# Kernel tuning notes

Measured on AMD Instinct MI355X. Metric: run time of the kernel, lower is better.

The kernel has to match this reference:

```python
import jax, jax.numpy as jnp
import numpy as np

THRESHOLD = 0.5
NEG_POS_RATIO = 3
ALPHA = 1.0
N_CLASSES = 81


def xy_to_cxcy(xy):
    return jnp.concatenate([(xy[..., :2] + xy[..., 2:]) / 2.0,
                            xy[..., 2:] - xy[..., :2]], axis=-1)


def cxcy_to_xy(cxcy):
    return jnp.concatenate([cxcy[..., :2] - cxcy[..., 2:] / 2.0,
                            cxcy[..., :2] + cxcy[..., 2:] / 2.0], axis=-1)


def cxcy_to_gcxgcy(cxcy, priors_cxcy):
    # SSD encoding with standard variances (0.1 for center, 0.2 for size)
    g_cxcy = (cxcy[..., :2] - priors_cxcy[..., :2]) / (priors_cxcy[..., 2:] / 10.0)
    g_wh = jnp.log(cxcy[..., 2:] / priors_cxcy[..., 2:]) * 5.0
    return jnp.concatenate([g_cxcy, g_wh], axis=-1)


def iou_pairwise(a_xy, b_xy):
    # a_xy: (N, O, 4), b_xy: (P, 4) -> (N, O, P)
    lt = jnp.maximum(a_xy[..., :, None, :2], b_xy[None, None, :, :2])
    rb = jnp.minimum(a_xy[..., :, None, 2:], b_xy[None, None, :, 2:])
    wh = jnp.clip(rb - lt, 0.0)
    inter = wh[..., 0] * wh[..., 1]
    area_a = (a_xy[..., 2] - a_xy[..., 0]) * (a_xy[..., 3] - a_xy[..., 1])
    area_b = (b_xy[:, 2] - b_xy[:, 0]) * (b_xy[:, 3] - b_xy[:, 1])
    union = area_a[..., :, None] + area_b[None, None, :] - inter
    return inter / union


def setup_inputs() -> dict:
    key = jax.random.key(0)
    k1, k2, k3, k4, k5, k6, k7 = jax.random.split(key, 7)
    N, P, C, O = 32, 8732, N_CLASSES, 16
    predicted_locs = jax.random.normal(k1, (N, P, 4), dtype=jnp.float32)
    predicted_scores = jax.random.normal(k2, (N, P, C), dtype=jnp.float32)
    # ground-truth boxes: build valid cxcy then convert to xy in [0, 1]
    b_cxy = jax.random.uniform(k3, (N, O, 2), minval=0.2, maxval=0.8)
    b_wh = jax.random.uniform(k4, (N, O, 2), minval=0.05, maxval=0.3)
    boxes = cxcy_to_xy(jnp.concatenate([b_cxy, b_wh], axis=-1)).astype(jnp.float32)
    labels = jax.random.randint(k5, (N, O), 1, C).astype(jnp.int32)  # 0 = background
    # priors in cxcy, valid (positive wh)
    p_cxy = jax.random.uniform(k6, (P, 2), minval=0.05, maxval=0.95)
    p_wh = jax.random.uniform(k7, (P, 2), minval=0.05, maxval=0.4)
    priors_cxcy = jnp.concatenate([p_cxy, p_wh], axis=-1).astype(jnp.float32)
    return {"predicted_locs": predicted_locs, "predicted_scores": predicted_scores,
            "boxes": boxes, "labels": labels, "priors_cxcy": priors_cxcy}


def reference(predicted_locs, predicted_scores, boxes, labels, priors_cxcy):
    N, P, C = predicted_scores.shape
    O = boxes.shape[1]
    priors_xy = cxcy_to_xy(priors_cxcy)  # (P, 4)

    overlap = iou_pairwise(boxes, priors_xy)            # (N, O, P)
    overlap_for_each_prior = overlap.max(axis=1)        # (N, P)
    object_for_each_prior = overlap.argmax(axis=1)      # (N, P)
    prior_for_each_object = overlap.argmax(axis=2)      # (N, O)

    obj_ids = jnp.arange(O)

    def assign(ofp, ovl, pfo):
        # force each object to be matched to its best prior with overlap 1
        ofp = ofp.at[pfo].set(obj_ids)
        ovl = ovl.at[pfo].set(1.0)
        return ofp, ovl

    object_for_each_prior, overlap_for_each_prior = jax.vmap(assign)(
        object_for_each_prior, overlap_for_each_prior, prior_for_each_object)

    label_for_each_prior = jnp.take_along_axis(labels, object_for_each_prior, axis=1)  # (N, P)
    true_classes = jnp.where(overlap_for_each_prior < THRESHOLD, 0, label_for_each_prior)

    matched_boxes = jnp.take_along_axis(
        boxes, object_for_each_prior[..., None], axis=1)  # (N, P, 4)
    true_locs = cxcy_to_gcxgcy(xy_to_cxcy(matched_boxes), priors_cxcy)

    positive = true_classes != 0                          # (N, P)
    pos_f = positive.astype(predicted_locs.dtype)

    # localization loss (L1, reduction='none' in original despite the name)
    loc_per_prior = jnp.abs(predicted_locs - true_locs).sum(axis=-1)  # (N, P)
    n_pos_total = pos_f.sum()
    loc_loss = (loc_per_prior * pos_f).sum() / (4.0 * n_pos_total)

    # confidence loss (cross entropy per prior)
    logp = jax.nn.log_softmax(predicted_scores, axis=-1)
    ce = -jnp.take_along_axis(logp, true_classes[..., None], axis=-1)[..., 0]  # (N, P)

    conf_loss_pos = (ce * pos_f).sum()
    ce_neg = jnp.where(positive, 0.0, ce)
    ce_neg_sorted = -jnp.sort(-ce_neg, axis=1)            # descending
    n_positives = positive.sum(axis=1)                    # (N,)
    hard = (jnp.arange(P)[None, :] < (NEG_POS_RATIO * n_positives)[:, None]).astype(ce.dtype)
    conf_loss_hard_neg = (ce_neg_sorted * hard).sum()
    conf_loss = (conf_loss_hard_neg + conf_loss_pos) / n_pos_total

    return conf_loss + ALPHA * loc_loss
```

## Files before the change

### kernel.cpp

```cpp
#include <hip/hip_runtime.h>
#include <hip/hip_bf16.h>
#include <stdint.h>

#define BLOCK 256
#define SBLOCK 128
#define MAXO 64
#define TK_THREADS 1024
#define CK_MAX 4096

__global__ void match_object_kernel(const float* __restrict__ boxes,
                                    const float* __restrict__ priors,
                                    int* __restrict__ pfop,
                                    float* __restrict__ acc, int* __restrict__ n_pos,
                                    unsigned* __restrict__ done, int N, int P, int O) {
    __shared__ unsigned long long swm[4];
    int idx = blockIdx.x, tid = threadIdx.x;
    if (idx == 0) {
        for (int j = tid; j < N; j += BLOCK) n_pos[j] = 0;
        if (tid >= 64 && tid < 67) acc[tid - 64] = 0.f;
        if (tid == 96) *done = 0u;
    }
    const float* b = boxes + (size_t)idx * 4;
    float bx0 = b[0], by0 = b[1], bx1 = b[2], by1 = b[3];
    float areaa = (bx1 - bx0) * (by1 - by0);

    unsigned long long best = 0ULL;
    for (int p = tid; p < P; p += BLOCK) {
        float4 pr = ((const float4*)priors)[p];
        float px0 = pr.x - pr.z * 0.5f, py0 = pr.y - pr.w * 0.5f;
        float px1 = pr.x + pr.z * 0.5f, py1 = pr.y + pr.w * 0.5f;
        float areab = (px1 - px0) * (py1 - py0);
        float ltx = fmaxf(bx0, px0), lty = fmaxf(by0, py0);
        float rbx = fminf(bx1, px1), rby = fminf(by1, py1);
        float wx = fmaxf(rbx - ltx, 0.f), wy = fmaxf(rby - lty, 0.f);
        float inter = wx * wy;
        float iou = inter / (areaa + areab - inter);
        unsigned long long cand = (((unsigned long long)__float_as_uint(iou)) << 32) |
                                  (unsigned long long)(0xFFFFFFFFu - (unsigned)p);
        if (cand > best) best = cand;
    }
    #pragma unroll
    for (int off = 32; off >= 1; off >>= 1) {
        unsigned long long other = __shfl_down(best, off);
        if (other > best) best = other;
    }
    if ((tid & 63) == 0) swm[tid >> 6] = best;
    __syncthreads();
    if (tid == 0) {
        unsigned long long r = swm[0];
        for (int w = 1; w < BLOCK / 64; ++w) if (swm[w] > r) r = swm[w];
        pfop[idx] = (int)(0xFFFFFFFFu - (unsigned)(r & 0xFFFFFFFFull));
    }
}

__global__ void __launch_bounds__(SBLOCK)
fused_staged_kernel(const float* __restrict__ boxes,
                    const float* __restrict__ priors,
                    const float* __restrict__ locs,
                    const int* __restrict__ labels,
                    const int* __restrict__ pfop,
                    const float* __restrict__ scores,
                    float* __restrict__ ce_neg,
                    float* __restrict__ pb_loc, float* __restrict__ pb_pce,
                    int* __restrict__ pb_npos,
                    int N, int P, int O) {
    __shared__ float4 sstage4[SBLOCK * 81 / 4];
    __shared__ float sbx[MAXO * 4];
    __shared__ int   spf[MAXO];
    __shared__ int   slab[MAXO];
    __shared__ float sl[2], sp[2]; __shared__ int sn[2];
    const float* sstage = (const float*)sstage4;

    int n = blockIdx.y, bx = blockIdx.x, tid = threadIdx.x;
    int w = tid >> 6, lane = tid & 63;
    int p0 = bx * SBLOCK;
    int rows = P - p0; if (rows > SBLOCK) rows = SBLOCK;
    int p = p0 + tid;
    bool valid = tid < rows;
    size_t t = (size_t)n * P + p;

    for (int i = tid; i < O * 4; i += SBLOCK) sbx[i] = boxes[(size_t)n * O * 4 + i];
    for (int i = tid; i < O; i += SBLOCK) { spf[i] = pfop[n * O + i]; slab[i] = labels[n * O + i]; }
    float4 pr = make_float4(0.f, 0.f, 1.f, 1.f);
    float4 pl = make_float4(0.f, 0.f, 0.f, 0.f);
    if (valid) {
        pr = ((const float4*)priors)[p];
        pl = ((const float4*)locs)[t];
    }

    const float4* chunk = (const float4*)(scores + ((size_t)n * P + p0) * 81);
    if (rows == SBLOCK) {
        #pragma unroll
        for (int j = 0; j < 20; ++j)
            sstage4[j * SBLOCK + tid] = chunk[j * SBLOCK + tid];
        if (tid < 32)
            sstage4[20 * SBLOCK + tid] = chunk[20 * SBLOCK + tid];
    } else {
        int nf4 = rows * 81 / 4;
        for (int j = 0; j < 21; ++j) {
            int idx = j * SBLOCK + tid;
            if (idx < nf4) sstage4[idx] = chunk[idx];
        }
    }
    __syncthreads();

    float my_loc = 0.f, my_pce = 0.f; int my_pos = 0;
    if (valid) {
        const float* row = sstage + tid * 81;
        float e = 0.f;
        #pragma unroll
        for (int j = 0; j < 81; ++j) e += __expf(row[j]);

        float px0 = pr.x - pr.z * 0.5f, py0 = pr.y - pr.w * 0.5f;
        float px1 = pr.x + pr.z * 0.5f, py1 = pr.y + pr.w * 0.5f;
        float areab = (px1 - px0) * (py1 - py0);
        float best = -1.f; int bo = 0;
        for (int o = 0; o < O; ++o) {
            float x0 = sbx[o*4+0], y0 = sbx[o*4+1], x1 = sbx[o*4+2], y1 = sbx[o*4+3];
            float ltx = fmaxf(x0, px0), lty = fmaxf(y0, py0);
            float rbx = fminf(x1, px1), rby = fminf(y1, py1);
            float wx = fmaxf(rbx - ltx, 0.f), wy = fmaxf(rby - lty, 0.f);
            float inter = wx * wy;
            float areao = (x1 - x0) * (y1 - y0);
            float iou = inter / (areao + areab - inter);
            if (iou > best) { best = iou; bo = o; }
        }
        int fo = -1;
        for (int o = 0; o < O; ++o) if (spf[o] == p) fo = o;
        int obj; float ov;
        if (fo >= 0) { obj = fo; ov = 1.0f; }
        else         { obj = bo; ov = best; }
        int tc = (ov < 0.5f) ? 0 : slab[obj];

        float stc = row[tc];
        float ce = logf(e) - stc;
        bool pos = (tc != 0);
        ce_neg[t] = pos ? 0.f : ce;
        if (pos) {
            my_pce = ce; my_pos = 1;
            float x0 = sbx[obj*4+0], y0 = sbx[obj*4+1], x1 = sbx[obj*4+2], y1 = sbx[obj*4+3];
            float cx = (x0 + x1) * 0.5f, cy = (y0 + y1) * 0.5f;
            float bw = x1 - x0, bh = y1 - y0;
            float g0 = (cx - pr.x) / (pr.z / 10.0f);
            float g1 = (cy - pr.y) / (pr.w / 10.0f);
            float g2 = logf(bw / pr.z) * 5.0f;
            float g3 = logf(bh / pr.w) * 5.0f;
            my_loc = fabsf(pl.x-g0) + fabsf(pl.y-g1) + fabsf(pl.z-g2) + fabsf(pl.w-g3);
        }
    }

    #pragma unroll
    for (int off = 32; off >= 1; off >>= 1) {
        my_loc += __shfl_down(my_loc, off);
        my_pce += __shfl_down(my_pce, off);
        my_pos += __shfl_down(my_pos, off);
    }
    if (lane == 0) { sl[w] = my_loc; sp[w] = my_pce; sn[w] = my_pos; }
    __syncthreads();
    if (tid == 0) {
        int npb = gridDim.x;
        pb_loc[n * npb + bx]  = sl[0] + sl[1];
        pb_pce[n * npb + bx]  = sp[0] + sp[1];
        pb_npos[n * npb + bx] = sn[0] + sn[1];
    }
}

__global__ void match_prior_kernel(const float* __restrict__ boxes,
                                   const float* __restrict__ priors,
                                   const float* __restrict__ locs,
                                   const int* __restrict__ labels,
                                   const int* __restrict__ pfop,
                                   int* __restrict__ tcarr,
                                   float* __restrict__ acc, int* __restrict__ n_pos,
                                   int N, int P, int O) {
    __shared__ float sbx[MAXO * 4];
    __shared__ float sarea[MAXO];
    __shared__ int   spf[MAXO];
    __shared__ int   slab[MAXO];
    int n = blockIdx.y, tid = threadIdx.x;
    if (tid < O * 4) sbx[tid] = boxes[(size_t)n * O * 4 + tid];
    if (tid >= 128 && tid < 128 + O) spf[tid - 128]  = pfop[n * O + (tid - 128)];
    if (tid >= 192 && tid < 192 + O) slab[tid - 192] = labels[n * O + (tid - 192)];
    __syncthreads();
    if (tid < O)
        sarea[tid] = (sbx[tid*4+2] - sbx[tid*4+0]) * (sbx[tid*4+3] - sbx[tid*4+1]);
    __syncthreads();

    int p = blockIdx.x * BLOCK + tid;
    bool valid = p < P;
    float my_loc = 0.f; int my_pos = 0;
    if (valid) {
        float4 pr = ((const float4*)priors)[p];
        float px0 = pr.x - pr.z * 0.5f, py0 = pr.y - pr.w * 0.5f;
        float px1 = pr.x + pr.z * 0.5f, py1 = pr.y + pr.w * 0.5f;
        float areab = (px1 - px0) * (py1 - py0);

        float best = -1.f; int bo = 0;
        for (int o = 0; o < O; ++o) {
            float ltx = fmaxf(sbx[o*4+0], px0);
            float lty = fmaxf(sbx[o*4+1], py0);
            float rbx = fminf(sbx[o*4+2], px1);
            float rby = fminf(sbx[o*4+3], py1);
            float wx = fmaxf(rbx - ltx, 0.f), wy = fmaxf(rby - lty, 0.f);
            float inter = wx * wy;
            float iou = inter / (sarea[o] + areab - inter);
            if (iou > best) { best = iou; bo = o; }
        }
        int fo = -1;
        for (int o = 0; o < O; ++o) if (spf[o] == p) fo = o;
        int obj; float ov;
        if (fo >= 0) { obj = fo; ov = 1.0f; }
        else         { obj = bo; ov = best; }
        int lab = slab[obj];
        int tc = (ov < 0.5f) ? 0 : lab;
        tcarr[(size_t)n * P + p] = tc;
        if (tc != 0) {
            my_pos = 1;
            float x0 = sbx[obj*4+0], y0 = sbx[obj*4+1], x1 = sbx[obj*4+2], y1 = sbx[obj*4+3];
            float cx = (x0 + x1) * 0.5f, cy = (y0 + y1) * 0.5f;
            float w = x1 - x0, h = y1 - y0;
            float g0 = (cx - pr.x) / (pr.z / 10.0f);
            float g1 = (cy - pr.y) / (pr.w / 10.0f);
            float g2 = logf(w / pr.z) * 5.0f;
            float g3 = logf(h / pr.w) * 5.0f;
            const float* pl = locs + ((size_t)n * P + p) * 4;
            my_loc = fabsf(pl[0]-g0) + fabsf(pl[1]-g1) + fabsf(pl[2]-g2) + fabsf(pl[3]-g3);
        }
    }
    #pragma unroll
    for (int off = 32; off >= 1; off >>= 1) {
        my_loc += __shfl_down(my_loc, off);
        my_pos += __shfl_down(my_pos, off);
    }
    if ((tid & 63) == 0 && my_pos) {
        atomicAdd(&acc[0], my_loc);
        atomicAdd(&n_pos[n], my_pos);
    }
}

__global__ void loss_generic_kernel(const float* __restrict__ scores,
                                    const int* __restrict__ tcarr,
                                    float* __restrict__ ce_neg, float* __restrict__ acc,
                                    int NP, int C) {
    int t = blockIdx.x * blockDim.x + threadIdx.x;
    if (t >= NP) return;
    int tc = tcarr[t];
    const float* s = scores + (size_t)t * C;
    float m = -3.0e38f;
    for (int j = 0; j < C; ++j) m = fmaxf(m, s[j]);
    float l = 0.f, stc = 0.f;
    for (int j = 0; j < C; ++j) {
        float v = s[j];
        l += __expf(v - m);
        if (j == tc) stc = v;
    }
    float ce = m + logf(l) - stc;
    bool pos = (tc != 0);
    ce_neg[t] = pos ? 0.f : ce;
    if (pos) atomicAdd(&acc[1], ce);
}

__global__ void topk_final_kernel(const float* __restrict__ ce_neg,
                                  int* __restrict__ n_pos,
                                  const float* __restrict__ pb_loc,
                                  const float* __restrict__ pb_pce,
                                  const int* __restrict__ pb_npos, int npb,
                                  float* __restrict__ acc, unsigned* __restrict__ done,
                                  int N, int P, unsigned* __restrict__ out) {
    __shared__ unsigned skeys[8732];
    __shared__ int hist[4096];
    __shared__ int part[1024];
    __shared__ int s_tb, s_ca, s_tb2, s_ca2, s_cnt, s_np;
    __shared__ float shf[16];
    int n = blockIdx.x, tid = threadIdx.x;

    int k;
    if (npb > 0) {
        if (tid < 64) {
            float psl = 0.f, psp = 0.f; int psn = 0;
            for (int i = tid; i < npb; i += 64) {
                psl += pb_loc[n * npb + i];
                psp += pb_pce[n * npb + i];
                psn += pb_npos[n * npb + i];
            }
            #pragma unroll
            for (int off = 32; off >= 1; off >>= 1) {
                psl += __shfl_down(psl, off);
                psp += __shfl_down(psp, off);
                psn += __shfl_down(psn, off);
            }
            if (tid == 0) {
                s_np = psn;
                n_pos[n] = psn;
                if (psl != 0.f) atomicAdd(&acc[0], psl);
                if (psp != 0.f) atomicAdd(&acc[1], psp);
            }
        }
        __syncthreads();
        k = 3 * s_np;
    } else {
        k = 3 * n_pos[n];
    }
    if (k > P) k = P;
    float bsum = 0.f;

    if (k > 0) {
        const float* row = ce_neg + (size_t)n * P;
        for (int i = tid; i < P; i += TK_THREADS) skeys[i] = __float_as_uint(row[i]);
        #pragma unroll
        for (int b = 0; b < 4; ++b) hist[tid * 4 + b] = 0;
        __syncthreads();

        for (int i = tid; i < P; i += TK_THREADS) atomicAdd(&hist[skeys[i] >> 20], 1);
        __syncthreads();
        int h0 = hist[tid*4], h1 = hist[tid*4+1], h2 = hist[tid*4+2], h3 = hist[tid*4+3];
        part[tid] = h0 + h1 + h2 + h3;
        __syncthreads();
        for (int s = 1; s < 1024; s <<= 1) {
            int v = part[tid] + ((tid + s < 1024) ? part[tid + s] : 0);
            __syncthreads();
            part[tid] = v;
            __syncthreads();
        }
        int sfx = (tid + 1 < 1024) ? part[tid + 1] : 0;
        int sf3 = sfx, sf2 = sfx + h3, sf1 = sf2 + h2, sf0 = sf1 + h1;
        if (sf0 < k && k <= sf0 + h0) { s_tb = tid*4;   s_ca = sf0; }
        if (sf1 < k && k <= sf1 + h1) { s_tb = tid*4+1; s_ca = sf1; }
        if (sf2 < k && k <= sf2 + h2) { s_tb = tid*4+2; s_ca = sf2; }
        if (sf3 < k && k <= sf3 + h3) { s_tb = tid*4+3; s_ca = sf3; }
        __syncthreads();
        int tb = s_tb, kk = k - s_ca;

        if (tid < 256) part[tid] = 0;
        __syncthreads();
        float ssum = 0.f;
        for (int i = tid; i < P; i += TK_THREADS) {
            unsigned key = skeys[i];
            int bin = key >> 20;
            if (bin > tb) ssum += __uint_as_float(key);
            else if (bin == tb) atomicAdd(&part[(key >> 12) & 255u], 1);
        }
        __syncthreads();
        if (tid < 256) {
            int cum = 0;
            for (int b = tid + 1; b < 256; ++b) cum += part[b];
            int h = part[tid];
            if (cum < kk && kk <= cum + h) { s_tb2 = tid; s_ca2 = cum; }
        }
        if (tid == 0) s_cnt = 0;
        __syncthreads();
        int tb2 = s_tb2, kk2 = kk - s_ca2;

        unsigned* ckeys = (unsigned*)hist;
        for (int i = tid; i < P; i += TK_THREADS) {
            unsigned key = skeys[i];
            if ((int)(key >> 20) == tb) {
                int b2 = (key >> 12) & 255u;
                if (b2 > tb2) ssum += __uint_as_float(key);
                else if (b2 == tb2) {
                    int slot = atomicAdd(&s_cnt, 1);
                    if (slot < CK_MAX) ckeys[slot] = key;
                }
            }
        }
        __syncthreads();
        int m = s_cnt; if (m > CK_MAX) m = CK_MAX;
        for (int i = tid; i < m; i += TK_THREADS) {
            unsigned key = ckeys[i];
            int rank = 0;
            for (int j = 0; j < m; ++j) {
                unsigned kj = ckeys[j];
                rank += (kj > key) || (kj == key && j < i);
            }
            if (rank < kk2) ssum += __uint_as_float(key);
        }
        #pragma unroll
        for (int off = 32; off >= 1; off >>= 1) ssum += __shfl_down(ssum, off);
        __syncthreads();
        if ((tid & 63) == 0) shf[tid >> 6] = ssum;
        __syncthreads();
        float tot = 0.f;
        for (int i = 0; i < 16; ++i) tot += shf[i];
        bsum = tot;
    }

    if (tid == 0) {
        if (bsum != 0.f) atomicAdd(&acc[2], bsum);
        __threadfence();
        unsigned old = atomicAdd(done, 1u);
        if (old == (unsigned)(N - 1)) {
            float a0 = atomicAdd(&acc[0], 0.f);
            float a1 = atomicAdd(&acc[1], 0.f);
            float a2 = atomicAdd(&acc[2], 0.f);
            int tot = 0;
            for (int i = 0; i < N; ++i) tot += n_pos[i];
            float npos = (float)tot;
            float conf = (a2 + a1) / npos;
            float loc  = a0 / (4.f * npos);
            float loss = conf + loc;
            unsigned ub = __float_as_uint(loss);
            unsigned r = (ub + 0x7FFFu + ((ub >> 16) & 1u)) >> 16;
            out[0] = (r << 16) | r;
        }
    }
}

extern "C" void kernel_launch(void* const* d_in, const int* in_sizes, int n_in,
                              void* d_out, int out_size, void* d_ws, size_t ws_size,
                              hipStream_t stream) {
    const float* locs   = (const float*)d_in[0];
    const float* scores = (const float*)d_in[1];
    const float* boxes  = (const float*)d_in[2];
    const int*   labels = (const int*)d_in[3];
    const float* priors = (const float*)d_in[4];

    int P = in_sizes[4] / 4;
    long long NPl = in_sizes[0] / 4;
    int N = (int)(NPl / P);
    int C = (int)((long long)in_sizes[1] / NPl);
    int O = in_sizes[3] / N;
    size_t NP = (size_t)N * P;
    int gx = (P + SBLOCK - 1) / SBLOCK;

    char* ws = (char*)d_ws;
    float*    acc    = (float*)ws;     ws += 16;
    unsigned* done   = (unsigned*)ws;  ws += 16;
    int*      n_pos  = (int*)ws;       ws += (size_t)N * 4;
    int*      pfop   = (int*)ws;       ws += (size_t)N * O * 4;
    float*    pb_loc = (float*)ws;     ws += (size_t)N * gx * 4;
    float*    pb_pce = (float*)ws;     ws += (size_t)N * gx * 4;
    int*      pb_npos= (int*)ws;       ws += (size_t)N * gx * 4;
    int*      tcarr  = (int*)ws;       ws += NP * 4;
    float*    ce_neg = (float*)ws;     ws += NP * 4;

    match_object_kernel<<<N * O, BLOCK, 0, stream>>>(boxes, priors, pfop, acc, n_pos,
                                                     done, N, P, O);
    int npb = 0;
    if (C == 81 && (P % 4) == 0 && O <= MAXO) {
        npb = gx;
        fused_staged_kernel<<<dim3(gx, N), SBLOCK, 0, stream>>>(
            boxes, priors, locs, labels, pfop, scores, ce_neg,
            pb_loc, pb_pce, pb_npos, N, P, O);
    } else {
        int gbx = (P + BLOCK - 1) / BLOCK;
        match_prior_kernel<<<dim3(gbx, N), BLOCK, 0, stream>>>(boxes, priors, locs, labels,
                                                               pfop, tcarr, acc, n_pos, N, P, O);
        loss_generic_kernel<<<(int)((NP + BLOCK - 1) / BLOCK), BLOCK, 0, stream>>>(
            scores, tcarr, ce_neg, acc, (int)NP, C);
    }
    topk_final_kernel<<<N, TK_THREADS, 0, stream>>>(ce_neg, n_pos,
                                                    pb_loc, pb_pce, pb_npos, npb,
                                                    acc, done, N, P, (unsigned*)d_out);
}
```

Measured before the change: 182.3 us.

## Build per-image radix histograms in fused kernel and shortcut top-k selection

The fused loss kernel now accumulates a per-image 4096-bin count and sum histogram of negative CE values with global atomics, zeroed in the matching kernel. The top-k kernel reads this histogram instead of loading all keys into shared memory and histogramming them. It finds the threshold bin from prefix sums, adds the bin sums above it, and only refines inside the threshold bin, using ballot-based compaction. This trades the top-k kernel's full-row pass for contended global atomics in the fused kernel plus extra zeroing traffic.

```diff
diff --git a/kernel.cpp b/kernel.cpp
--- a/kernel.cpp
+++ b/kernel.cpp
@@ -7,12 +7,16 @@
 #define MAXO 64
 #define TK_THREADS 1024
 #define CK_MAX 4096
+#define NBIN 4096
 
 __global__ void match_object_kernel(const float* __restrict__ boxes,
                                     const float* __restrict__ priors,
                                     int* __restrict__ pfop,
                                     float* __restrict__ acc, int* __restrict__ n_pos,
-                                    unsigned* __restrict__ done, int N, int P, int O) {
+                                    unsigned* __restrict__ done,
+                                    int* __restrict__ hzero,
+                                    long long hlen,
+                                    int N, int P, int O) {
     __shared__ unsigned long long swm[4];
     int idx = blockIdx.x, tid = threadIdx.x;
     if (idx == 0) {
@@ -20,6 +24,10 @@
         if (tid >= 64 && tid < 67) acc[tid - 64] = 0.f;
         if (tid == 96) *done = 0u;
     }
+    for (long long j = (long long)idx * BLOCK + tid; j < hlen;
+         j += (long long)gridDim.x * BLOCK)
+        hzero[j] = 0;
+
     const float* b = boxes + (size_t)idx * 4;
     float bx0 = b[0], by0 = b[1], bx1 = b[2], by1 = b[3];
     float areaa = (bx1 - bx0) * (by1 - by0);
@@ -63,6 +71,7 @@
                     float* __restrict__ ce_neg,
                     float* __restrict__ pb_loc, float* __restrict__ pb_pce,
                     int* __restrict__ pb_npos,
+                    int* __restrict__ hcnt, float* __restrict__ hsum,
                     int N, int P, int O) {
     __shared__ float4 sstage4[SBLOCK * 81 / 4];
     __shared__ float sbx[MAXO * 4];
@@ -135,7 +144,12 @@
         float stc = row[tc];
         float ce = logf(e) - stc;
         bool pos = (tc != 0);
-        ce_neg[t] = pos ? 0.f : ce;
+        float cv = pos ? 0.f : ce;
+        ce_neg[t] = cv;
+        unsigned key = __float_as_uint(cv);
+        int bin = (int)(key >> 20);
+        atomicAdd(&hcnt[n * NBIN + bin], 1);
+        atomicAdd(&hsum[n * NBIN + bin], cv);
         if (pos) {
             my_pce = ce; my_pos = 1;
             float x0 = sbx[obj*4+0], y0 = sbx[obj*4+1], x1 = sbx[obj*4+2], y1 = sbx[obj*4+3];
@@ -265,14 +279,19 @@
                                   const float* __restrict__ pb_loc,
                                   const float* __restrict__ pb_pce,
                                   const int* __restrict__ pb_npos, int npb,
+                                  const int* __restrict__ hcnt,
+                                  const float* __restrict__ hsum,
                                   float* __restrict__ acc, unsigned* __restrict__ done,
                                   int N, int P, unsigned* __restrict__ out) {
     __shared__ unsigned skeys[8732];
     __shared__ int hist[4096];
     __shared__ int part[1024];
-    __shared__ int s_tb, s_ca, s_tb2, s_ca2, s_cnt, s_np;
+    __shared__ int wtot[16]; __shared__ float wtotf[16];
+    __shared__ int s_tb, s_ca, s_tb2, s_ca2, s_cnt, s_np, s_htb;
+    __shared__ float s_b0, s_ftb;
     __shared__ float shf[16];
     int n = blockIdx.x, tid = threadIdx.x;
+    int w = tid >> 6, lane = tid & 63;
 
     int k;
     if (npb > 0) {
@@ -304,13 +323,113 @@
     if (k > P) k = P;
     float bsum = 0.f;
 
-    if (k > 0) {
+    if (k > 0 && npb > 0) {
+        int b0 = tid * 4;
+        int4   hc = *(const int4*)&hcnt[(size_t)n * NBIN + b0];
+        float4 hf = *(const float4*)&hsum[(size_t)n * NBIN + b0];
+        int   lc = hc.x + hc.y + hc.z + hc.w;
+        float lf = hf.x + hf.y + hf.z + hf.w;
+        int si = lc; float sf = lf;
+        #pragma unroll
+        for (int off = 1; off < 64; off <<= 1) {
+            int ti = __shfl(si, lane + off);
+            float tf = __shfl(sf, lane + off);
+            if (lane + off < 64) { si += ti; sf += tf; }
+        }
+        if (lane == 0) { wtot[w] = si; wtotf[w] = sf; }
+        __syncthreads();
+        if (tid < 16) {
+            int ov = wtot[tid]; float ovf = wtotf[tid];
+            int v = ov; float vf = ovf;
+            #pragma unroll
+            for (int off = 1; off < 16; off <<= 1) {
+                int tv = __shfl(v, lane + off);
+                float tvf = __shfl(vf, lane + off);
+                if (lane + off < 16) { v += tv; vf += tvf; }
+            }
+            wtot[tid] = v - ov; wtotf[tid] = vf - ovf;
+        }
+        if (tid == 0) s_cnt = 0;
+        __syncthreads();
+        int   after  = wtot[w] + (si - lc);
+        float afterf = wtotf[w] + (sf - lf);
+        int sf3 = after,       sf2 = sf3 + hc.w, sf1 = sf2 + hc.z, sf0 = sf1 + hc.y;
+        float ff3 = afterf,    ff2 = ff3 + hf.w, ff1 = ff2 + hf.z, ff0 = ff1 + hf.y;
+        if (sf0 < k && k <= sf0 + hc.x) { s_tb = b0;   s_ca = sf0; s_b0 = ff0; s_htb = hc.x; s_ftb = hf.x; }
+        if (sf1 < k && k <= sf1 + hc.y) { s_tb = b0+1; s_ca = sf1; s_b0 = ff1; s_htb = hc.y; s_ftb = hf.y; }
+        if (sf2 < k && k <= sf2 + hc.z) { s_tb = b0+2; s_ca = sf2; s_b0 = ff2; s_htb = hc.z; s_ftb = hf.z; }
+        if (sf3 < k && k <= sf3 + hc.w) { s_tb = b0+3; s_ca = sf3; s_b0 = ff3; s_htb = hc.w; s_ftb = hf.w; }
+        __syncthreads();
+        int tb = s_tb, kk = k - s_ca;
+        bool shortcut = (kk == s_htb);
+        float ssum = 0.f;
+
+        if (!shortcut) {
+            unsigned* ckeys = (unsigned*)hist;
+            const float* row = ce_neg + (size_t)n * P;
+            for (int i = tid; i < P; i += TK_THREADS) {
+                unsigned key = __float_as_uint(row[i]);
+                bool pred = (int)(key >> 20) == tb;
+                unsigned long long bal = __ballot(pred);
+                if (bal) {
+                    int ldr = __builtin_ctzll(bal);
+                    int base = 0;
+                    if (lane == ldr) base = atomicAdd(&s_cnt, __builtin_popcountll(bal));
+                    base = __shfl(base, ldr);
+                    if (pred) {
+                        int slot = base + __builtin_popcountll(bal & ((1ull << lane) - 1ull));
+                        if (slot < CK_MAX) ckeys[slot] = key;
+                    }
+                }
+            }
+            __syncthreads();
+            int m = s_cnt; if (m > CK_MAX) m = CK_MAX;
+
+            if (tid < 256) part[tid] = 0;
+            __syncthreads();
+            for (int i = tid; i < m; i += TK_THREADS)
+                atomicAdd(&part[(ckeys[i] >> 12) & 255u], 1);
+            __syncthreads();
+            if (tid < 256) {
+                int cum = 0;
+                for (int b2 = tid + 1; b2 < 256; ++b2) cum += part[b2];
+                int h = part[tid];
+                if (cum < kk && kk <= cum + h) { s_tb2 = tid; s_ca2 = cum; }
+            }
+            __syncthreads();
+            int tb2 = s_tb2, kk2 = kk - s_ca2;
+
+            for (int i = tid; i < m; i += TK_THREADS) {
+                unsigned key = ckeys[i];
+                int b2 = (key >> 12) & 255u;
+                if (b2 > tb2) ssum += __uint_as_float(key);
+                else if (b2 == tb2) {
+                    int rank = 0;
+                    for (int j = 0; j < m; ++j) {
+                        unsigned kj = ckeys[j];
+                        if (((kj >> 12) & 255u) == (unsigned)tb2)
+                            rank += (kj > key) || (kj == key && j < i);
+                    }
+                    if (rank < kk2) ssum += __uint_as_float(key);
+                }
+            }
+        }
+        #pragma unroll
+        for (int off = 32; off >= 1; off >>= 1) ssum += __shfl_down(ssum, off);
+        __syncthreads();
+        if ((tid & 63) == 0) shf[tid >> 6] = ssum;
+        __syncthreads();
+        if (tid == 0) {
+            float tot = 0.f;
+            for (int i = 0; i < 16; ++i) tot += shf[i];
+            bsum = tot + s_b0 + (shortcut ? s_ftb : 0.f);
+        }
+    } else if (k > 0) {
         const float* row = ce_neg + (size_t)n * P;
         for (int i = tid; i < P; i += TK_THREADS) skeys[i] = __float_as_uint(row[i]);
         #pragma unroll
         for (int b = 0; b < 4; ++b) hist[tid * 4 + b] = 0;
         __syncthreads();
-
         for (int i = tid; i < P; i += TK_THREADS) atomicAdd(&hist[skeys[i] >> 20], 1);
         __syncthreads();
         int h0 = hist[tid*4], h1 = hist[tid*4+1], h2 = hist[tid*4+2], h3 = hist[tid*4+3];
@@ -330,7 +449,6 @@
         if (sf3 < k && k <= sf3 + h3) { s_tb = tid*4+3; s_ca = sf3; }
         __syncthreads();
         int tb = s_tb, kk = k - s_ca;
-
         if (tid < 256) part[tid] = 0;
         __syncthreads();
         float ssum = 0.f;
@@ -350,7 +468,6 @@
         if (tid == 0) s_cnt = 0;
         __syncthreads();
         int tb2 = s_tb2, kk2 = kk - s_ca2;
-
         unsigned* ckeys = (unsigned*)hist;
         for (int i = tid; i < P; i += TK_THREADS) {
             unsigned key = skeys[i];
@@ -379,9 +496,11 @@
         __syncthreads();
         if ((tid & 63) == 0) shf[tid >> 6] = ssum;
         __syncthreads();
-        float tot = 0.f;
-        for (int i = 0; i < 16; ++i) tot += shf[i];
-        bsum = tot;
+        if (tid == 0) {
+            float tot = 0.f;
+            for (int i = 0; i < 16; ++i) tot += shf[i];
+            bsum = tot;
+        }
     }
 
     if (tid == 0) {
@@ -427,20 +546,23 @@
     unsigned* done   = (unsigned*)ws;  ws += 16;
     int*      n_pos  = (int*)ws;       ws += (size_t)N * 4;
     int*      pfop   = (int*)ws;       ws += (size_t)N * O * 4;
+    int*      hcnt   = (int*)ws;       ws += (size_t)N * NBIN * 4;
+    float*    hsum   = (float*)ws;     ws += (size_t)N * NBIN * 4;
     float*    pb_loc = (float*)ws;     ws += (size_t)N * gx * 4;
     float*    pb_pce = (float*)ws;     ws += (size_t)N * gx * 4;
     int*      pb_npos= (int*)ws;       ws += (size_t)N * gx * 4;
     int*      tcarr  = (int*)ws;       ws += NP * 4;
     float*    ce_neg = (float*)ws;     ws += NP * 4;
 
+    long long hlen = (long long)N * NBIN * 2;
     match_object_kernel<<<N * O, BLOCK, 0, stream>>>(boxes, priors, pfop, acc, n_pos,
-                                                     done, N, P, O);
+                                                     done, hcnt, hlen, N, P, O);
     int npb = 0;
     if (C == 81 && (P % 4) == 0 && O <= MAXO) {
         npb = gx;
         fused_staged_kernel<<<dim3(gx, N), SBLOCK, 0, stream>>>(
             boxes, priors, locs, labels, pfop, scores, ce_neg,
-            pb_loc, pb_pce, pb_npos, N, P, O);
+            pb_loc, pb_pce, pb_npos, hcnt, hsum, N, P, O);
     } else {
         int gbx = (P + BLOCK - 1) / BLOCK;
         match_prior_kernel<<<dim3(gbx, N), BLOCK, 0, stream>>>(boxes, priors, locs, labels,
@@ -450,5 +572,6 @@
     }
     topk_final_kernel<<<N, TK_THREADS, 0, stream>>>(ce_neg, n_pos,
                                                     pb_loc, pb_pce, pb_npos, npb,
+                                                    hcnt, hsum,
                                                     acc, done, N, P, (unsigned*)d_out);
 }
```

Result: slower. 364.3 us (+99.9%).

## Drop object-matching kernel; patch forced prior matches in top-k kernel

Applied to the files above, without the earlier changes.

Removes the separate per-object best-prior kernel from the fast path. The fused per-prior kernel now assigns classes from the best-IoU object alone and runs at 64 threads per block. The top-k kernel recomputes each object's best prior with one wave per object and applies correction deltas to the per-image loc, positive CE, positive count and ce_neg keys. This removes a launch and a dependency, at the cost of serial work inside the 32-block top-k kernel and a limit of O<=16 on the fast path.

```diff
diff --git a/kernel.cpp b/kernel.cpp
--- a/kernel.cpp
+++ b/kernel.cpp
@@ -3,7 +3,7 @@
 #include <stdint.h>
 
 #define BLOCK 256
-#define SBLOCK 128
+#define FB 64
 #define MAXO 64
 #define TK_THREADS 1024
 #define CK_MAX 4096
@@ -53,34 +53,35 @@
     }
 }
 
-__global__ void __launch_bounds__(SBLOCK)
+__global__ void __launch_bounds__(FB)
 fused_staged_kernel(const float* __restrict__ boxes,
                     const float* __restrict__ priors,
                     const float* __restrict__ locs,
                     const int* __restrict__ labels,
-                    const int* __restrict__ pfop,
                     const float* __restrict__ scores,
                     float* __restrict__ ce_neg,
                     float* __restrict__ pb_loc, float* __restrict__ pb_pce,
                     int* __restrict__ pb_npos,
+                    float* __restrict__ acc, unsigned* __restrict__ done,
                     int N, int P, int O) {
-    __shared__ float4 sstage4[SBLOCK * 81 / 4];
+    __shared__ float4 sstage4[FB * 81 / 4];
     __shared__ float sbx[MAXO * 4];
-    __shared__ int   spf[MAXO];
     __shared__ int   slab[MAXO];
-    __shared__ float sl[2], sp[2]; __shared__ int sn[2];
     const float* sstage = (const float*)sstage4;
 
     int n = blockIdx.y, bx = blockIdx.x, tid = threadIdx.x;
-    int w = tid >> 6, lane = tid & 63;
-    int p0 = bx * SBLOCK;
-    int rows = P - p0; if (rows > SBLOCK) rows = SBLOCK;
+    if (bx == 0 && n == 0) {
+        if (tid < 3) acc[tid] = 0.f;
+        if (tid == 3) *done = 0u;
+    }
+    int p0 = bx * FB;
+    int rows = P - p0; if (rows > FB) rows = FB;
     int p = p0 + tid;
     bool valid = tid < rows;
     size_t t = (size_t)n * P + p;
 
-    for (int i = tid; i < O * 4; i += SBLOCK) sbx[i] = boxes[(size_t)n * O * 4 + i];
-    for (int i = tid; i < O; i += SBLOCK) { spf[i] = pfop[n * O + i]; slab[i] = labels[n * O + i]; }
+    for (int i = tid; i < O * 4; i += FB) sbx[i] = boxes[(size_t)n * O * 4 + i];
+    for (int i = tid; i < O; i += FB) slab[i] = labels[n * O + i];
     float4 pr = make_float4(0.f, 0.f, 1.f, 1.f);
     float4 pl = make_float4(0.f, 0.f, 0.f, 0.f);
     if (valid) {
@@ -89,16 +90,16 @@
     }
 
     const float4* chunk = (const float4*)(scores + ((size_t)n * P + p0) * 81);
-    if (rows == SBLOCK) {
+    if (rows == FB) {
         #pragma unroll
         for (int j = 0; j < 20; ++j)
-            sstage4[j * SBLOCK + tid] = chunk[j * SBLOCK + tid];
-        if (tid < 32)
-            sstage4[20 * SBLOCK + tid] = chunk[20 * SBLOCK + tid];
+            sstage4[j * FB + tid] = chunk[j * FB + tid];
+        if (tid < 16)
+            sstage4[20 * FB + tid] = chunk[20 * FB + tid];
     } else {
         int nf4 = rows * 81 / 4;
         for (int j = 0; j < 21; ++j) {
-            int idx = j * SBLOCK + tid;
+            int idx = j * FB + tid;
             if (idx < nf4) sstage4[idx] = chunk[idx];
         }
     }
@@ -125,12 +126,7 @@
             float iou = inter / (areao + areab - inter);
             if (iou > best) { best = iou; bo = o; }
         }
-        int fo = -1;
-        for (int o = 0; o < O; ++o) if (spf[o] == p) fo = o;
-        int obj; float ov;
-        if (fo >= 0) { obj = fo; ov = 1.0f; }
-        else         { obj = bo; ov = best; }
-        int tc = (ov < 0.5f) ? 0 : slab[obj];
+        int tc = (best < 0.5f) ? 0 : slab[bo];
 
         float stc = row[tc];
         float ce = logf(e) - stc;
@@ -138,7 +134,7 @@
         ce_neg[t] = pos ? 0.f : ce;
         if (pos) {
             my_pce = ce; my_pos = 1;
-            float x0 = sbx[obj*4+0], y0 = sbx[obj*4+1], x1 = sbx[obj*4+2], y1 = sbx[obj*4+3];
+            float x0 = sbx[bo*4+0], y0 = sbx[bo*4+1], x1 = sbx[bo*4+2], y1 = sbx[bo*4+3];
             float cx = (x0 + x1) * 0.5f, cy = (y0 + y1) * 0.5f;
             float bw = x1 - x0, bh = y1 - y0;
             float g0 = (cx - pr.x) / (pr.z / 10.0f);
@@ -155,13 +151,11 @@
         my_pce += __shfl_down(my_pce, off);
         my_pos += __shfl_down(my_pos, off);
     }
-    if (lane == 0) { sl[w] = my_loc; sp[w] = my_pce; sn[w] = my_pos; }
-    __syncthreads();
     if (tid == 0) {
         int npb = gridDim.x;
-        pb_loc[n * npb + bx]  = sl[0] + sl[1];
-        pb_pce[n * npb + bx]  = sp[0] + sp[1];
-        pb_npos[n * npb + bx] = sn[0] + sn[1];
+        pb_loc[n * npb + bx]  = my_loc;
+        pb_pce[n * npb + bx]  = my_pce;
+        pb_npos[n * npb + bx] = my_pos;
     }
 }
 
@@ -265,17 +259,33 @@
                                   const float* __restrict__ pb_loc,
                                   const float* __restrict__ pb_pce,
                                   const int* __restrict__ pb_npos, int npb,
+                                  const float* __restrict__ boxes,
+                                  const float* __restrict__ priors,
+                                  const float* __restrict__ locs,
+                                  const int* __restrict__ labels,
+                                  const float* __restrict__ scores,
                                   float* __restrict__ acc, unsigned* __restrict__ done,
-                                  int N, int P, unsigned* __restrict__ out) {
+                                  int N, int P, int O, unsigned* __restrict__ out) {
     __shared__ unsigned skeys[8732];
     __shared__ int hist[4096];
     __shared__ int part[1024];
+    __shared__ float sbx_l[64];
+    __shared__ int   slab_l[16];
+    __shared__ int   spf_l[16];
+    __shared__ float sdl[16], sdp[16]; __shared__ int sdn[16];
+    __shared__ float s_psl, s_psp; __shared__ int s_psn;
     __shared__ int s_tb, s_ca, s_tb2, s_ca2, s_cnt, s_np;
     __shared__ float shf[16];
     int n = blockIdx.x, tid = threadIdx.x;
+    int w = tid >> 6, lane = tid & 63;
 
     int k;
     if (npb > 0) {
+        const float* rowg = ce_neg + (size_t)n * P;
+        for (int i = tid; i < P; i += TK_THREADS) skeys[i] = __float_as_uint(rowg[i]);
+        if (tid < O * 4) sbx_l[tid] = boxes[(size_t)n * O * 4 + tid];
+        if (tid >= 64 && tid < 64 + O) slab_l[tid - 64] = labels[n * O + (tid - 64)];
+        if (tid >= 128 && tid < 144) { sdl[tid-128] = 0.f; sdp[tid-128] = 0.f; sdn[tid-128] = 0; }
         if (tid < 64) {
             float psl = 0.f, psp = 0.f; int psn = 0;
             for (int i = tid; i < npb; i += 64) {
@@ -289,12 +299,119 @@
                 psp += __shfl_down(psp, off);
                 psn += __shfl_down(psn, off);
             }
-            if (tid == 0) {
-                s_np = psn;
-                n_pos[n] = psn;
-                if (psl != 0.f) atomicAdd(&acc[0], psl);
-                if (psp != 0.f) atomicAdd(&acc[1], psp);
-            }
+            if (tid == 0) { s_psl = psl; s_psp = psp; s_psn = psn; }
+        }
+        __syncthreads();
+
+        if (w < O) {
+            float bx0 = sbx_l[w*4+0], by0 = sbx_l[w*4+1];
+            float bx1 = sbx_l[w*4+2], by1 = sbx_l[w*4+3];
+            float areaa = (bx1 - bx0) * (by1 - by0);
+            unsigned long long best = 0ULL;
+            for (int p = lane; p < P; p += 64) {
+                float4 pr = ((const float4*)priors)[p];
+                float px0 = pr.x - pr.z * 0.5f, py0 = pr.y - pr.w * 0.5f;
+                float px1 = pr.x + pr.z * 0.5f, py1 = pr.y + pr.w * 0.5f;
+                float areab = (px1 - px0) * (py1 - py0);
+                float ltx = fmaxf(bx0, px0), lty = fmaxf(by0, py0);
+                float rbx = fminf(bx1, px1), rby = fminf(by1, py1);
+                float wx = fmaxf(rbx - ltx, 0.f), wy = fmaxf(rby - lty, 0.f);
+                float inter = wx * wy;
+                float iou = inter / (areaa + areab - inter);
+                unsigned long long cand = (((unsigned long long)__float_as_uint(iou)) << 32) |
+                                          (unsigned long long)(0xFFFFFFFFu - (unsigned)p);
+                if (cand > best) best = cand;
+            }
+            #pragma unroll
+            for (int off = 32; off >= 1; off >>= 1) {
+                unsigned long long o2 = __shfl_down(best, off);
+                if (o2 > best) best = o2;
+            }
+            if (lane == 0) spf_l[w] = (int)(0xFFFFFFFFu - (unsigned)(best & 0xFFFFFFFFull));
+        }
+        __syncthreads();
+
+        if (w < O) {
+            int pstar = spf_l[w];
+            bool skip = false;
+            for (int o2 = w + 1; o2 < O; ++o2) if (spf_l[o2] == pstar) skip = true;
+            if (!skip) {
+                size_t tstar = (size_t)n * P + pstar;
+                float4 prs = ((const float4*)priors)[pstar];
+                float px0 = prs.x - prs.z * 0.5f, py0 = prs.y - prs.w * 0.5f;
+                float px1 = prs.x + prs.z * 0.5f, py1 = prs.y + prs.w * 0.5f;
+                float areab = (px1 - px0) * (py1 - py0);
+                unsigned long long bkey = 0ULL;
+                if (lane < O) {
+                    float x0 = sbx_l[lane*4+0], y0 = sbx_l[lane*4+1];
+                    float x1 = sbx_l[lane*4+2], y1 = sbx_l[lane*4+3];
+                    float ltx = fmaxf(x0, px0), lty = fmaxf(y0, py0);
+                    float rbx = fminf(x1, px1), rby = fminf(y1, py1);
+                    float wx = fmaxf(rbx - ltx, 0.f), wy = fmaxf(rby - lty, 0.f);
+                    float inter = wx * wy;
+                    float areao = (x1 - x0) * (y1 - y0);
+                    float iou = inter / (areao + areab - inter);
+                    bkey = (((unsigned long long)__float_as_uint(iou)) << 32) |
+                           (unsigned long long)(0xFFFFFFFFu - (unsigned)lane);
+                }
+                #pragma unroll
+                for (int off = 32; off >= 1; off >>= 1) {
+                    unsigned long long o2 = __shfl_down(bkey, off);
+                    if (o2 > bkey) bkey = o2;
+                }
+                const float* srow = scores + tstar * 81;
+                float e = __expf(srow[lane]);
+                if (lane < 17) e += __expf(srow[64 + lane]);
+                #pragma unroll
+                for (int off = 32; off >= 1; off >>= 1) e += __shfl_xor(e, off);
+                if (lane == 0) {
+                    int bo = (int)(0xFFFFFFFFu - (unsigned)(bkey & 0xFFFFFFFFull));
+                    float ov = __uint_as_float((unsigned)(bkey >> 32));
+                    int tc_base = (ov < 0.5f) ? 0 : slab_l[bo];
+                    int lab = slab_l[w];
+                    float l = logf(e);
+                    float4 plv = ((const float4*)locs)[tstar];
+                    auto locof = [&](int obj) {
+                        float x0 = sbx_l[obj*4+0], y0 = sbx_l[obj*4+1];
+                        float x1 = sbx_l[obj*4+2], y1 = sbx_l[obj*4+3];
+                        float cx = (x0 + x1) * 0.5f, cy = (y0 + y1) * 0.5f;
+                        float bw2 = x1 - x0, bh2 = y1 - y0;
+                        float g0 = (cx - prs.x) / (prs.z / 10.0f);
+                        float g1 = (cy - prs.y) / (prs.w / 10.0f);
+                        float g2 = logf(bw2 / prs.z) * 5.0f;
+                        float g3 = logf(bh2 / prs.w) * 5.0f;
+                        return fabsf(plv.x-g0)+fabsf(plv.y-g1)+fabsf(plv.z-g2)+fabsf(plv.w-g3);
+                    };
+                    if (lab != 0) {
+                        float ce_new = l - srow[lab];
+                        float ln = locof(w);
+                        if (tc_base != 0) {
+                            float ce_old = l - srow[tc_base];
+                            float lo = locof(bo);
+                            sdl[w] = ln - lo; sdp[w] = ce_new - ce_old; sdn[w] = 0;
+                        } else {
+                            skeys[pstar] = 0u;
+                            sdl[w] = ln; sdp[w] = ce_new; sdn[w] = 1;
+                        }
+                    } else if (tc_base != 0) {
+                        float ce_old = l - srow[tc_base];
+                        float lo = locof(bo);
+                        skeys[pstar] = __float_as_uint(l - srow[0]);
+                        sdl[w] = -lo; sdp[w] = -ce_old; sdn[w] = -1;
+                    }
+                }
+            }
+        }
+        __syncthreads();
+        if (tid == 0) {
+            float dl = 0.f, dp = 0.f; int dn = 0;
+            for (int i = 0; i < 16; ++i) { dl += sdl[i]; dp += sdp[i]; dn += sdn[i]; }
+            int np2 = s_psn + dn;
+            s_np = np2;
+            n_pos[n] = np2;
+            float a0v = s_psl + dl, a1v = s_psp + dp;
+            if (a0v != 0.f) atomicAdd(&acc[0], a0v);
+            if (a1v != 0.f) atomicAdd(&acc[1], a1v);
         }
         __syncthreads();
         k = 3 * s_np;
@@ -305,8 +422,10 @@
     float bsum = 0.f;
 
     if (k > 0) {
-        const float* row = ce_neg + (size_t)n * P;
-        for (int i = tid; i < P; i += TK_THREADS) skeys[i] = __float_as_uint(row[i]);
+        if (npb == 0) {
+            const float* row = ce_neg + (size_t)n * P;
+            for (int i = tid; i < P; i += TK_THREADS) skeys[i] = __float_as_uint(row[i]);
+        }
         #pragma unroll
         for (int b = 0; b < 4; ++b) hist[tid * 4 + b] = 0;
         __syncthreads();
@@ -420,7 +539,7 @@
     int C = (int)((long long)in_sizes[1] / NPl);
     int O = in_sizes[3] / N;
     size_t NP = (size_t)N * P;
-    int gx = (P + SBLOCK - 1) / SBLOCK;
+    int gx = (P + FB - 1) / FB;
 
     char* ws = (char*)d_ws;
     float*    acc    = (float*)ws;     ws += 16;
@@ -433,15 +552,15 @@
     int*      tcarr  = (int*)ws;       ws += NP * 4;
     float*    ce_neg = (float*)ws;     ws += NP * 4;
 
-    match_object_kernel<<<N * O, BLOCK, 0, stream>>>(boxes, priors, pfop, acc, n_pos,
-                                                     done, N, P, O);
     int npb = 0;
-    if (C == 81 && (P % 4) == 0 && O <= MAXO) {
+    if (C == 81 && (P % 4) == 0 && O <= 16) {
         npb = gx;
-        fused_staged_kernel<<<dim3(gx, N), SBLOCK, 0, stream>>>(
-            boxes, priors, locs, labels, pfop, scores, ce_neg,
-            pb_loc, pb_pce, pb_npos, N, P, O);
+        fused_staged_kernel<<<dim3(gx, N), FB, 0, stream>>>(
+            boxes, priors, locs, labels, scores, ce_neg,
+            pb_loc, pb_pce, pb_npos, acc, done, N, P, O);
     } else {
+        match_object_kernel<<<N * O, BLOCK, 0, stream>>>(boxes, priors, pfop, acc, n_pos,
+                                                         done, N, P, O);
         int gbx = (P + BLOCK - 1) / BLOCK;
         match_prior_kernel<<<dim3(gbx, N), BLOCK, 0, stream>>>(boxes, priors, locs, labels,
                                                                pfop, tcarr, acc, n_pos, N, P, O);
@@ -450,5 +569,6 @@
     }
     topk_final_kernel<<<N, TK_THREADS, 0, stream>>>(ce_neg, n_pos,
                                                     pb_loc, pb_pce, pb_npos, npb,
-                                                    acc, done, N, P, (unsigned*)d_out);
+                                                    boxes, priors, locs, labels, scores,
+                                                    acc, done, N, P, O, (unsigned*)d_out);
 }
```

Measured after the change: 205.6 us. +12.8%, slower.
